# Kernel tuning notes

Measured on AMD Instinct MI355X. Metric: run time of the kernel, lower is better.

Reference implementation:

```python
import jax, jax.numpy as jnp
import numpy as np

EPS = 1e-5

def _conv(x, w, pad):
    # NCHW conv, stride 1, no bias
    return jax.lax.conv_general_dilated(x, w, (1, 1), [(pad, pad), (pad, pad)],
                                        dimension_numbers=('NCHW', 'OIHW', 'NCHW'))

def _bn(x, g, b, m, v):
    # inference-mode BatchNorm2d folded to scale/shift
    s = g * jax.lax.rsqrt(v + EPS)
    return x * s[None, :, None, None] + (b - m * s)[None, :, None, None]

def _cbr(x, w, g, b, m, v):
    # convolution helper module: 3x3 conv (pad 1, no bias) + BN + ReLU
    return jax.nn.relu(_bn(_conv(x, w, 1), g, b, m, v))


def setup_inputs() -> dict:
    key = jax.random.key(0)
    ks = iter(jax.random.split(key, 40))
    dim, mid, B, H, W = 256, 128, 4, 128, 128
    def conv_w(shape):
        fan = shape[1] * shape[2] * shape[3]
        return jax.random.normal(next(ks), shape, jnp.float32) / np.float32(np.sqrt(fan))
    def bn_p(c):
        return (jax.random.normal(next(ks), (c,), jnp.float32) * 0.1 + 1.0,
                jax.random.normal(next(ks), (c,), jnp.float32) * 0.1,
                jax.random.normal(next(ks), (c,), jnp.float32) * 0.1,
                jax.random.uniform(next(ks), (c,), jnp.float32, 0.5, 1.5))
    x = jax.random.normal(next(ks), (B, dim, H, W), jnp.float32)
    w_p1 = conv_w((mid, dim, 3, 3)); g_p1, b_p1, m_p1, v_p1 = bn_p(mid)
    w_p2 = conv_w((mid, dim, 3, 3)); g_p2, b_p2, m_p2, v_p2 = bn_p(mid)
    w_pc = conv_w((dim, mid, 3, 3)); g_pb, b_pb, m_pb, v_pb = bn_p(dim)
    w_c1 = conv_w((dim, dim, 1, 1)); g_b1, b_b1, m_b1, v_b1 = bn_p(dim)
    w_c2 = conv_w((dim, dim, 3, 3)); g_c2, b_c2, m_c2, v_c2 = bn_p(dim)
    return dict(x=x,
                w_p1=w_p1, g_p1=g_p1, b_p1=b_p1, m_p1=m_p1, v_p1=v_p1,
                w_p2=w_p2, g_p2=g_p2, b_p2=b_p2, m_p2=m_p2, v_p2=v_p2,
                w_pc=w_pc, g_pb=g_pb, b_pb=b_pb, m_pb=m_pb, v_pb=v_pb,
                w_c1=w_c1, g_b1=g_b1, b_b1=b_b1, m_b1=m_b1, v_b1=v_b1,
                w_c2=w_c2, g_c2=g_c2, b_c2=b_c2, m_c2=m_c2, v_c2=v_c2)


def reference(x, w_p1, g_p1, b_p1, m_p1, v_p1,
              w_p2, g_p2, b_p2, m_p2, v_p2,
              w_pc, g_pb, b_pb, m_pb, v_pb,
              w_c1, g_b1, b_b1, m_b1, v_b1,
              w_c2, g_c2, b_c2, m_c2, v_c2):
    p1 = _cbr(x, w_p1, g_p1, b_p1, m_p1, v_p1)          # [B,128,H,W]
    top = jax.lax.cummax(p1, axis=2, reverse=True)       # TopPool: max over rows below
    p2 = _cbr(x, w_p2, g_p2, b_p2, m_p2, v_p2)          # [B,128,H,W]
    left = jax.lax.cummax(p2, axis=3, reverse=True)      # LeftPool: max over cols to the right
    p_bn1 = _bn(_conv(top + left, w_pc, 1), g_pb, b_pb, m_pb, v_pb)  # [B,dim,H,W]
    bn1 = _bn(_conv(x, w_c1, 0), g_b1, b_b1, m_b1, v_b1)             # 1x1 skip branch
    relu1 = jax.nn.relu(p_bn1 + bn1)
    return _cbr(relu1, w_c2, g_c2, b_c2, m_c2, v_c2)
```

## Files before the change

kernel.cpp:

```cpp
#include <hip/hip_runtime.h>
#include <hip/hip_bf16.h>

#define HH 128
#define WW 128
#define BB 4
#define NPIX 16384
#define EPSV 1e-5f

using bfrag = __attribute__((ext_vector_type(8))) short;
using f32x4 = __attribute__((ext_vector_type(4))) float;
using us8   = __attribute__((ext_vector_type(8))) unsigned short;

__device__ __forceinline__ float bf2f(ushort u) {
  union { unsigned int i; float f; } x; x.i = ((unsigned int)u) << 16; return x.f;
}
__device__ __forceinline__ ushort f2bf(float f) {
  union { float f; unsigned int i; } x; x.f = f;
  unsigned int r = x.i + 0x7fffu + ((x.i >> 16) & 1u);
  return (ushort)(r >> 16);
}

#define GLOAD16(gsrc, ldst) \
  __builtin_amdgcn_global_load_lds( \
      (const __attribute__((address_space(1))) unsigned int*)(gsrc), \
      (__attribute__((address_space(3))) unsigned int*)(ldst), 16, 0, 0)

template<int CIN1, int TAPS1, int CIN2, int TAPS2, int EPI>
__global__ __launch_bounds__(512, 2)
void convgemm(const ushort* __restrict__ B1,
              const ushort* __restrict__ B2,
              const ushort* __restrict__ wR,
              const float*  __restrict__ tb,
              const float*  __restrict__ tb2,
              void*          __restrict__ outp,
              const ushort* __restrict__ zerop)
{
  __shared__ char ldsb[131072];
  constexpr int nch1 = CIN1 / 64;
  constexpr int nch2 = (CIN2 > 0) ? CIN2 / 64 : 0;
  constexpr int NCH  = TAPS1 * nch1 + TAPS2 * nch2;

  const int nid = (blockIdx.x & 7) * 32 + (blockIdx.x >> 3);
  const int b   = nid >> 6;
  const int h2  = (nid & 63) * 2;

  const int tid  = threadIdx.x;
  const int lane = tid & 63;
  const int wid  = tid >> 6;
  const int wc   = wid & 3;
  const int m0   = (wid >> 2) * 128;
  const int n0   = wc * 64;

  f32x4 acc[8][4];
  #pragma unroll
  for (int i = 0; i < 8; ++i)
    #pragma unroll
    for (int j = 0; j < 4; ++j) acc[i][j] = (f32x4){0.f, 0.f, 0.f, 0.f};

  const int sl8 = (((tid & 7) ^ ((tid >> 3) & 7)) << 3);
  int ro1[4], ro2[4], w_[4], prow_[4];
  #pragma unroll
  for (int s = 0; s < 4; ++s) {
    const int rowB = s * 64 + (tid >> 3);
    prow_[s] = rowB >> 7;
    w_[s]    = rowB & 127;
    ro1[s]   = (prow_[s] * WW + w_[s]) * CIN1 + sl8;
    ro2[s]   = (CIN2 > 0) ? rowB * CIN2 + sl8 : 0;
  }
  const size_t B1base = (size_t)b * NPIX * CIN1;
  const size_t B2base = (CIN2 > 0) ? (size_t)b * NPIX * CIN2 : 0;

  auto stageB = [&](int t, int buf) {
    char* base = ldsb + buf * 65536 + 32768;
    if (CIN2 == 0 || t < TAPS1 * nch1) {
      const int tap = t / nch1, ch = t - tap * nch1;
      const int dy = (TAPS1 == 9) ? tap / 3 - 1 : 0;
      const int dx = (TAPS1 == 9) ? tap - (tap / 3) * 3 - 1 : 0;
      const int hy0 = h2 + dy;
      const bool oob0 = (hy0 < 0) | (hy0 > 127);
      const bool oob1 = (hy0 + 1 < 0) | (hy0 + 1 > 127);
      const int zr = (dx < 0) ? 0 : ((dx > 0) ? 127 : -1);
      const ushort* bch = B1 + B1base + (size_t)(hy0 * WW + dx) * CIN1 + ch * 64;
      #pragma unroll
      for (int s = 0; s < 4; ++s) {
        const bool bad = (prow_[s] ? oob1 : oob0) || (w_[s] == zr);
        const ushort* src = bad ? zerop : (bch + ro1[s]);
        GLOAD16(src, base + s * 8192 + tid * 16);
      }
    } else {
      const int ch = t - TAPS1 * nch1;
      const ushort* bch = B2 + B2base + (size_t)(h2 * WW) * CIN2 + ch * 64;
      #pragma unroll
      for (int s = 0; s < 4; ++s)
        GLOAD16(bch + ro2[s], base + s * 8192 + tid * 16);
    }
  };

  auto stageA = [&](int t, int buf) {
    char* base = ldsb + buf * 65536;
    const char* wsrc = (const char*)(wR + (size_t)t * (256 * 64));
    GLOAD16(wsrc + 0 * 8192 + tid * 16, base + 0 * 8192 + tid * 16);
    GLOAD16(wsrc + 2 * 8192 + tid * 16, base + 2 * 8192 + tid * 16);
    GLOAD16(wsrc + 1 * 8192 + tid * 16, base + 1 * 8192 + tid * 16);
    GLOAD16(wsrc + 3 * 8192 + tid * 16, base + 3 * 8192 + tid * 16);
  };

  stageB(0, 0);
  stageA(0, 0);
  int cur = 0;
  for (int t = 0; t < NCH; ++t) {
    const char* cbase = ldsb + cur * 65536;
    asm volatile("s_waitcnt vmcnt(2)" ::: "memory");
    __builtin_amdgcn_s_barrier();
    __builtin_amdgcn_sched_barrier(0);
    bfrag bf[2][4], af[2][4];
    #pragma unroll
    for (int kc = 0; kc < 2; ++kc) {
      const int sw = ((((kc << 2) | (lane >> 4)) ^ (lane & 7)) << 4);
      #pragma unroll
      for (int nf = 0; nf < 4; ++nf)
        bf[kc][nf] = *(const bfrag*)(cbase + 32768 +
                        (n0 + nf * 16 + (lane & 15)) * 128 + sw);
      #pragma unroll
      for (int mf = 0; mf < 4; ++mf)
        af[kc][mf] = *(const bfrag*)(cbase +
                        (m0 + mf * 16 + (lane & 15)) * 128 + sw);
    }
    if (t + 1 < NCH) stageB(t + 1, cur ^ 1);
    __builtin_amdgcn_s_setprio(1);
    #pragma unroll
    for (int kc = 0; kc < 2; ++kc)
      #pragma unroll
      for (int mf = 0; mf < 4; ++mf)
        #pragma unroll
        for (int nf = 0; nf < 4; ++nf)
          acc[mf][nf] = __builtin_amdgcn_mfma_f32_16x16x32_bf16(
              af[kc][mf], bf[kc][nf], acc[mf][nf], 0, 0, 0);
    __builtin_amdgcn_s_setprio(0);
    __builtin_amdgcn_sched_barrier(0);
    if (t + 1 < NCH) asm volatile("s_waitcnt vmcnt(4)" ::: "memory");
    else             asm volatile("s_waitcnt vmcnt(0)" ::: "memory");
    __builtin_amdgcn_s_barrier();
    __builtin_amdgcn_sched_barrier(0);
    bfrag ag[2][4];
    #pragma unroll
    for (int kc = 0; kc < 2; ++kc) {
      const int sw = ((((kc << 2) | (lane >> 4)) ^ (lane & 7)) << 4);
      #pragma unroll
      for (int mf = 0; mf < 4; ++mf)
        ag[kc][mf] = *(const bfrag*)(cbase +
                        (m0 + 64 + mf * 16 + (lane & 15)) * 128 + sw);
    }
    if (t + 1 < NCH) stageA(t + 1, cur ^ 1);
    __builtin_amdgcn_s_setprio(1);
    #pragma unroll
    for (int kc = 0; kc < 2; ++kc)
      #pragma unroll
      for (int mf = 0; mf < 4; ++mf)
        #pragma unroll
        for (int nf = 0; nf < 4; ++nf)
          acc[4 + mf][nf] = __builtin_amdgcn_mfma_f32_16x16x32_bf16(
              ag[kc][mf], bf[kc][nf], acc[4 + mf][nf], 0, 0, 0);
    __builtin_amdgcn_s_setprio(0);
    __builtin_amdgcn_sched_barrier(0);
    cur ^= 1;
  }

  if (EPI == 4) {
    ushort* ct = (ushort*)ldsb;
    #pragma unroll
    for (int ph = 0; ph < 2; ++ph) {
      __syncthreads();
      if ((wc >> 1) == ph) {
        const int lp0 = (wc & 1) * 64 + (lane & 15);
        #pragma unroll
        for (int mf = 0; mf < 8; ++mf) {
          #pragma unroll
          for (int r2 = 0; r2 < 4; ++r2) {
            const int o = m0 + mf * 16 + (lane >> 4) * 4 + r2;
            const float bias = tb[o] + tb2[o];
            #pragma unroll
            for (int nf = 0; nf < 4; ++nf)
              ct[(lp0 + nf * 16) * 264 + o] =
                  f2bf(fmaxf(acc[mf][nf][r2] + bias, 0.f));
          }
        }
      }
      __syncthreads();
      const int lp = tid >> 2;
      const int q  = tid & 3;
      ushort* dst = (ushort*)outp +
          ((size_t)b * NPIX + (h2 + ph) * WW + lp) * 256 + q * 64;
      const ushort* src = ct + lp * 264 + q * 64;
      #pragma unroll
      for (int j = 0; j < 8; ++j)
        *(us8*)(dst + j * 8) = *(const us8*)(src + j * 8);
    }
    return;
  }

  const int prow = wc >> 1;
  const int hout = h2 + prow;
  const int wbase = (wc & 1) * 64 + (lane & 15);
  #pragma unroll
  for (int mf = 0; mf < 8; ++mf) {
    #pragma unroll
    for (int r2 = 0; r2 < 4; ++r2) {
      const int o = m0 + mf * 16 + (lane >> 4) * 4 + r2;
      const float bias = tb[o];
      #pragma unroll
      for (int nf = 0; nf < 4; ++nf) {
        const int w = wbase + nf * 16;
        float v = fmaxf(acc[mf][nf][r2] + bias, 0.f);
        const size_t oi = (((size_t)(b * 256 + o)) << 14) + hout * WW + w;
        if (EPI == 0) ((ushort*)outp)[oi] = f2bf(v);
        else          ((float*)outp)[oi] = v;
      }
    }
  }
}

struct WSeg {
  const float *W, *g, *bb, *mm, *vv;
  ushort* dst; float* tb;
  int CIN, COUT, TAPS, o_off, cb, start, end;
};

__device__ __forceinline__ void wrepack_one(const WSeg& s, int e) {
  const int tap = e % s.TAPS;
  const int ci  = (e / s.TAPS) % s.CIN;
  const int o   = e / (s.TAPS * s.CIN);
  const int oi  = o + s.o_off;
  const float sc = s.g[o] * rsqrtf(s.vv[o] + EPSV);
  const int nch = s.CIN / 64;
  const int ch = ci >> 6, kl = ci & 63;
  const int slot = (kl >> 3) ^ (oi & 7);
  s.dst[(((size_t)((s.cb + tap * nch + ch) * s.COUT) + oi) << 6) +
        (slot << 3) + (kl & 7)] = f2bf(s.W[e] * sc);
  if (ci == 0 && tap == 0) s.tb[oi] = s.bb[o] - s.mm[o] * sc;
}

__global__ __launch_bounds__(256)
void wrepack_all(WSeg s0, WSeg s1, WSeg s2, WSeg s3, WSeg s4) {
  const int id = blockIdx.x * 256 + threadIdx.x;
  if (id < s0.end)      wrepack_one(s0, id - s0.start);
  else if (id < s1.end) wrepack_one(s1, id - s1.start);
  else if (id < s2.end) wrepack_one(s2, id - s2.start);
  else if (id < s3.end) wrepack_one(s3, id - s3.start);
  else if (id < s4.end) wrepack_one(s4, id - s4.start);
}

__global__ __launch_bounds__(256)
void repack_x(const float* __restrict__ x, ushort* __restrict__ xT)
{
  const int b  = blockIdx.z;
  const int cq = threadIdx.x >> 6;
  const int pg = threadIdx.x & 63;
  const int p0 = blockIdx.x * 256 + pg * 4;
  const size_t xb = (size_t)b * 256 * NPIX;
  ushort* ob = xT + ((size_t)b * NPIX + p0) * 256 + cq * 64;
  for (int cc = 0; cc < 64; cc += 8) {
    us8 v[4];
    #pragma unroll
    for (int j = 0; j < 8; ++j) {
      const float4 q = *(const float4*)&x[xb + (size_t)(cq * 64 + cc + j) * NPIX + p0];
      v[0][j] = f2bf(q.x); v[1][j] = f2bf(q.y);
      v[2][j] = f2bf(q.z); v[3][j] = f2bf(q.w);
    }
    #pragma unroll
    for (int k = 0; k < 4; ++k)
      *(us8*)(ob + (size_t)k * 256 + cc) = v[k];
  }
}

__global__ __launch_bounds__(256)
void sum_repack(const ushort* __restrict__ p12, ushort* __restrict__ sT)
{
  const int b  = blockIdx.z;
  const int cq = threadIdx.x >> 6;
  const int pg = threadIdx.x & 63;
  const int p0 = blockIdx.x * 256 + pg * 4;
  const size_t base = (size_t)b * 256 * NPIX;
  const ushort* P1 = p12 + base;
  const ushort* P2 = p12 + base + (size_t)128 * NPIX;
  ushort* ob = sT + ((size_t)b * NPIX + p0) * 128 + cq * 32;
  for (int cc = 0; cc < 32; cc += 8) {
    us8 v[4];
    #pragma unroll
    for (int j = 0; j < 8; ++j) {
      const size_t ci = (size_t)(cq * 32 + cc + j) * NPIX + p0;
      const ushort4 a = *(const ushort4*)&P1[ci];
      const ushort4 d = *(const ushort4*)&P2[ci];
      v[0][j] = f2bf(bf2f(a.x) + bf2f(d.x));
      v[1][j] = f2bf(bf2f(a.y) + bf2f(d.y));
      v[2][j] = f2bf(bf2f(a.z) + bf2f(d.z));
      v[3][j] = f2bf(bf2f(a.w) + bf2f(d.w));
    }
    #pragma unroll
    for (int k = 0; k < 4; ++k)
      *(us8*)(ob + (size_t)k * 128 + cc) = v[k];
  }
}

__global__ __launch_bounds__(256)
void scans(ushort* __restrict__ p)
{
  const int bid = blockIdx.x;
  if (bid < 256) {
    const int b = bid >> 6;
    const int c = (bid & 63) * 2 + (threadIdx.x >> 7);
    const int w = threadIdx.x & 127;
    ushort* base = p + ((size_t)(b * 256 + c)) * NPIX + w;
    float cur = bf2f(base[(HH - 1) * WW]);
    for (int hr = HH - 2; hr >= 0; --hr) {
      cur = fmaxf(cur, bf2f(base[hr * WW]));
      base[hr * WW] = f2bf(cur);
    }
  } else {
    const int lane = threadIdx.x & 63;
    const int rid  = (bid - 256) * 4 + (threadIdx.x >> 6);
    const int b = rid >> 14;
    const int rem = rid & 16383;
    const int c = rem >> 7, h = rem & 127;
    ushort* r = p + ((size_t)(b * 256 + 128 + c)) * NPIX + h * WW;
    const ushort2 u = ((const ushort2*)r)[lane];
    const float e0 = bf2f(u.x), e1 = bf2f(u.y);
    float m = fmaxf(e0, e1);
    #pragma unroll
    for (int off = 1; off < 64; off <<= 1) {
      const float o = __shfl_down(m, off, 64);
      if (lane + off < 64) m = fmaxf(m, o);
    }
    float s = __shfl_down(m, 1, 64);
    if (lane == 63) s = -3.4e38f;
    const float o1 = fmaxf(e1, s);
    const float o0 = fmaxf(e0, o1);
    ushort2 w2; w2.x = f2bf(o0); w2.y = f2bf(o1);
    ((ushort2*)r)[lane] = w2;
  }
}

extern "C" void kernel_launch(void* const* d_in, const int* in_sizes, int n_in,
                              void* d_out, int out_size, void* d_ws, size_t ws_size,
                              hipStream_t stream) {
  const float* x    = (const float*)d_in[0];
  const float* w_p1 = (const float*)d_in[1];
  const float* g_p1 = (const float*)d_in[2];
  const float* b_p1 = (const float*)d_in[3];
  const float* m_p1 = (const float*)d_in[4];
  const float* v_p1 = (const float*)d_in[5];
  const float* w_p2 = (const float*)d_in[6];
  const float* g_p2 = (const float*)d_in[7];
  const float* b_p2 = (const float*)d_in[8];
  const float* m_p2 = (const float*)d_in[9];
  const float* v_p2 = (const float*)d_in[10];
  const float* w_pc = (const float*)d_in[11];
  const float* g_pb = (const float*)d_in[12];
  const float* b_pb = (const float*)d_in[13];
  const float* m_pb = (const float*)d_in[14];
  const float* v_pb = (const float*)d_in[15];
  const float* w_c1 = (const float*)d_in[16];
  const float* g_b1 = (const float*)d_in[17];
  const float* b_b1 = (const float*)d_in[18];
  const float* m_b1 = (const float*)d_in[19];
  const float* v_b1 = (const float*)d_in[20];
  const float* w_c2 = (const float*)d_in[21];
  const float* g_c2 = (const float*)d_in[22];
  const float* b_c2 = (const float*)d_in[23];
  const float* m_c2 = (const float*)d_in[24];
  const float* v_c2 = (const float*)d_in[25];

  char* ws = (char*)d_ws;
  ushort* xT      = (ushort*)(ws + 0);
  ushort* p12     = (ushort*)(ws + 33554432);
  ushort* relu1T  = (ushort*)(ws + 33554432);
  ushort* sumT    = (ushort*)(ws + 67108864);
  ushort* wR_p12  = (ushort*)(ws + 100663296);
  ushort* wR_pcc1 = (ushort*)(ws + 101842944);
  ushort* wR_c2   = (ushort*)(ws + 102563840);
  float*  tb_p12  = (float*)(ws + 103743488);
  float*  tb_pc   = (float*)(ws + 103744512);
  float*  tb_c1   = (float*)(ws + 103745536);
  float*  tb_c2   = (float*)(ws + 103746560);
  ushort* zerop   = (ushort*)(ws + 103747584);

  hipMemsetAsync(zerop, 0, 256, stream);

  const int n_p  = 128 * 256 * 9;
  const int n_pc = 256 * 128 * 9;
  const int n_c1 = 256 * 256 * 1;
  const int n_c2 = 256 * 256 * 9;
  WSeg s0 = {w_p1, g_p1, b_p1, m_p1, v_p1, wR_p12, tb_p12, 256, 256, 9, 0, 0,
             0, n_p};
  WSeg s1 = {w_p2, g_p2, b_p2, m_p2, v_p2, wR_p12, tb_p12, 256, 256, 9, 128, 0,
             n_p, 2 * n_p};
  WSeg s2 = {w_pc, g_pb, b_pb, m_pb, v_pb, wR_pcc1, tb_pc, 128, 256, 9, 0, 0,
             2 * n_p, 2 * n_p + n_pc};
  WSeg s3 = {w_c1, g_b1, b_b1, m_b1, v_b1, wR_pcc1, tb_c1, 256, 256, 1, 0, 18,
             2 * n_p + n_pc, 2 * n_p + n_pc + n_c1};
  WSeg s4 = {w_c2, g_c2, b_c2, m_c2, v_c2, wR_c2, tb_c2, 256, 256, 9, 0, 0,
             2 * n_p + n_pc + n_c1, 2 * n_p + n_pc + n_c1 + n_c2};
  const int n_all = 2 * n_p + n_pc + n_c1 + n_c2;
  wrepack_all<<<dim3((n_all + 255) / 256), 256, 0, stream>>>(s0, s1, s2, s3, s4);

  repack_x<<<dim3(NPIX / 256, 1, BB), 256, 0, stream>>>(x, xT);

  convgemm<256, 9, 0, 0, 0><<<dim3(256), 512, 0, stream>>>(
      xT, nullptr, wR_p12, tb_p12, nullptr, p12, zerop);

  scans<<<dim3(256 + 16384), 256, 0, stream>>>(p12);

  sum_repack<<<dim3(NPIX / 256, 1, BB), 256, 0, stream>>>(p12, sumT);

  convgemm<128, 9, 256, 1, 4><<<dim3(256), 512, 0, stream>>>(
      sumT, xT, wR_pcc1, tb_pc, tb_c1, relu1T, zerop);

  convgemm<256, 9, 0, 0, 3><<<dim3(256), 512, 0, stream>>>(
      relu1T, nullptr, wR_c2, tb_c2, nullptr, (void*)d_out, zerop);
}
```

Before: 287.1 us.

## Split GEMM main loop into four phases with finer-grained interleaved prefetch

The per-chunk loop is restructured from two halves into four phases (A-half by k-chunk). Each phase reads only the LDS fragments it needs and issues half of the next chunk's global-to-LDS staging between phases. Wait counts are retuned so each phase waits only on the segments it reads. The intent is to overlap global loads with MFMA work more evenly and cut register pressure from holding fragments. The cost is more barriers per iteration, and the correctness of the vmcnt accounting depends on the order in which segments are loaded.

```diff
diff --git a/kernel.cpp b/kernel.cpp
--- a/kernel.cpp
+++ b/kernel.cpp
@@ -70,7 +70,7 @@
   const size_t B1base = (size_t)b * NPIX * CIN1;
   const size_t B2base = (CIN2 > 0) ? (size_t)b * NPIX * CIN2 : 0;
 
-  auto stageB = [&](int t, int buf) {
+  auto stageB = [&](int t, int buf, int part) {
     char* base = ldsb + buf * 65536 + 32768;
     if (CIN2 == 0 || t < TAPS1 * nch1) {
       const int tap = t / nch1, ch = t - tap * nch1;
@@ -82,7 +82,8 @@
       const int zr = (dx < 0) ? 0 : ((dx > 0) ? 127 : -1);
       const ushort* bch = B1 + B1base + (size_t)(hy0 * WW + dx) * CIN1 + ch * 64;
       #pragma unroll
-      for (int s = 0; s < 4; ++s) {
+      for (int si = 0; si < 2; ++si) {
+        const int s = part * 2 + si;
         const bool bad = (prow_[s] ? oob1 : oob0) || (w_[s] == zr);
         const ushort* src = bad ? zerop : (bch + ro1[s]);
         GLOAD16(src, base + s * 8192 + tid * 16);
@@ -91,80 +92,95 @@
       const int ch = t - TAPS1 * nch1;
       const ushort* bch = B2 + B2base + (size_t)(h2 * WW) * CIN2 + ch * 64;
       #pragma unroll
-      for (int s = 0; s < 4; ++s)
+      for (int si = 0; si < 2; ++si) {
+        const int s = part * 2 + si;
         GLOAD16(bch + ro2[s], base + s * 8192 + tid * 16);
+      }
     }
   };
 
-  auto stageA = [&](int t, int buf) {
+  auto stageA = [&](int t, int buf, int part) {
     char* base = ldsb + buf * 65536;
     const char* wsrc = (const char*)(wR + (size_t)t * (256 * 64));
-    GLOAD16(wsrc + 0 * 8192 + tid * 16, base + 0 * 8192 + tid * 16);
-    GLOAD16(wsrc + 2 * 8192 + tid * 16, base + 2 * 8192 + tid * 16);
-    GLOAD16(wsrc + 1 * 8192 + tid * 16, base + 1 * 8192 + tid * 16);
-    GLOAD16(wsrc + 3 * 8192 + tid * 16, base + 3 * 8192 + tid * 16);
+    const int sa = part, sb = part + 2;
+    GLOAD16(wsrc + sa * 8192 + tid * 16, base + sa * 8192 + tid * 16);
+    GLOAD16(wsrc + sb * 8192 + tid * 16, base + sb * 8192 + tid * 16);
   };
 
-  stageB(0, 0);
-  stageA(0, 0);
+#define READ_A(dst_, mfh_, kc_) do { \
+    const int sw_ = ((((kc_) << 2) | (lane >> 4)) ^ (lane & 7)) << 4; \
+    _Pragma("unroll") \
+    for (int mf_ = 0; mf_ < 4; ++mf_) \
+      dst_[mf_] = *(const bfrag*)(cbase + \
+          (m0 + (mfh_) * 64 + mf_ * 16 + (lane & 15)) * 128 + sw_); \
+  } while (0)
+
+#define READ_B(dst_, kc_) do { \
+    const int sw_ = ((((kc_) << 2) | (lane >> 4)) ^ (lane & 7)) << 4; \
+    _Pragma("unroll") \
+    for (int nf_ = 0; nf_ < 4; ++nf_) \
+      dst_[nf_] = *(const bfrag*)(cbase + 32768 + \
+          (n0 + nf_ * 16 + (lane & 15)) * 128 + sw_); \
+  } while (0)
+
+#define MFMA16(rb_, A_, B_) do { \
+    __builtin_amdgcn_s_setprio(1); \
+    _Pragma("unroll") \
+    for (int mf_ = 0; mf_ < 4; ++mf_) \
+      _Pragma("unroll") \
+      for (int nf_ = 0; nf_ < 4; ++nf_) \
+        acc[(rb_) + mf_][nf_] = __builtin_amdgcn_mfma_f32_16x16x32_bf16( \
+            A_[mf_], B_[nf_], acc[(rb_) + mf_][nf_], 0, 0, 0); \
+    __builtin_amdgcn_s_setprio(0); \
+  } while (0)
+
+  stageB(0, 0, 0);
+  stageB(0, 0, 1);
+  stageA(0, 0, 0);
+  stageA(0, 0, 1);
   int cur = 0;
   for (int t = 0; t < NCH; ++t) {
     const char* cbase = ldsb + cur * 65536;
-    asm volatile("s_waitcnt vmcnt(2)" ::: "memory");
-    __builtin_amdgcn_s_barrier();
-    __builtin_amdgcn_sched_barrier(0);
-    bfrag bf[2][4], af[2][4];
-    #pragma unroll
-    for (int kc = 0; kc < 2; ++kc) {
-      const int sw = ((((kc << 2) | (lane >> 4)) ^ (lane & 7)) << 4);
-      #pragma unroll
-      for (int nf = 0; nf < 4; ++nf)
-        bf[kc][nf] = *(const bfrag*)(cbase + 32768 +
-                        (n0 + nf * 16 + (lane & 15)) * 128 + sw);
-      #pragma unroll
-      for (int mf = 0; mf < 4; ++mf)
-        af[kc][mf] = *(const bfrag*)(cbase +
-                        (m0 + mf * 16 + (lane & 15)) * 128 + sw);
-    }
-    if (t + 1 < NCH) stageB(t + 1, cur ^ 1);
-    __builtin_amdgcn_s_setprio(1);
-    #pragma unroll
-    for (int kc = 0; kc < 2; ++kc)
-      #pragma unroll
-      for (int mf = 0; mf < 4; ++mf)
-        #pragma unroll
-        for (int nf = 0; nf < 4; ++nf)
-          acc[mf][nf] = __builtin_amdgcn_mfma_f32_16x16x32_bf16(
-              af[kc][mf], bf[kc][nf], acc[mf][nf], 0, 0, 0);
-    __builtin_amdgcn_s_setprio(0);
-    __builtin_amdgcn_sched_barrier(0);
-    if (t + 1 < NCH) asm volatile("s_waitcnt vmcnt(4)" ::: "memory");
-    else             asm volatile("s_waitcnt vmcnt(0)" ::: "memory");
-    __builtin_amdgcn_s_barrier();
-    __builtin_amdgcn_sched_barrier(0);
-    bfrag ag[2][4];
-    #pragma unroll
-    for (int kc = 0; kc < 2; ++kc) {
-      const int sw = ((((kc << 2) | (lane >> 4)) ^ (lane & 7)) << 4);
-      #pragma unroll
-      for (int mf = 0; mf < 4; ++mf)
-        ag[kc][mf] = *(const bfrag*)(cbase +
-                        (m0 + 64 + mf * 16 + (lane & 15)) * 128 + sw);
-    }
-    if (t + 1 < NCH) stageA(t + 1, cur ^ 1);
-    __builtin_amdgcn_s_setprio(1);
-    #pragma unroll
-    for (int kc = 0; kc < 2; ++kc)
-      #pragma unroll
-      for (int mf = 0; mf < 4; ++mf)
-        #pragma unroll
-        for (int nf = 0; nf < 4; ++nf)
-          acc[4 + mf][nf] = __builtin_amdgcn_mfma_f32_16x16x32_bf16(
-              ag[kc][mf], bf[kc][nf], acc[4 + mf][nf], 0, 0, 0);
-    __builtin_amdgcn_s_setprio(0);
-    __builtin_amdgcn_sched_barrier(0);
+    const bool pf = (t + 1 < NCH);
+    if (pf) stageB(t + 1, cur ^ 1, 0);
+    if (pf) asm volatile("s_waitcnt vmcnt(4)" ::: "memory");
+    else    asm volatile("s_waitcnt vmcnt(2)" ::: "memory");
+    __builtin_amdgcn_s_barrier();
+    __builtin_amdgcn_sched_barrier(0);
+    bfrag bf0[4], af0[4];
+    READ_B(bf0, 0);
+    READ_A(af0, 0, 0);
+    __builtin_amdgcn_sched_barrier(0);
+    __builtin_amdgcn_s_barrier();
+    MFMA16(0, af0, bf0);
+    if (pf) stageB(t + 1, cur ^ 1, 1);
+    if (pf) asm volatile("s_waitcnt vmcnt(4)" ::: "memory");
+    else    asm volatile("s_waitcnt vmcnt(0)" ::: "memory");
+    __builtin_amdgcn_s_barrier();
+    __builtin_amdgcn_sched_barrier(0);
+    bfrag af1[4];
+    READ_A(af1, 1, 0);
+    __builtin_amdgcn_sched_barrier(0);
+    __builtin_amdgcn_s_barrier();
+    MFMA16(4, af1, bf0);
+    if (pf) stageA(t + 1, cur ^ 1, 0);
+    bfrag bf1[4], af2[4];
+    READ_B(bf1, 1);
+    READ_A(af2, 0, 1);
+    __builtin_amdgcn_sched_barrier(0);
+    __builtin_amdgcn_s_barrier();
+    MFMA16(0, af2, bf1);
+    if (pf) stageA(t + 1, cur ^ 1, 1);
+    bfrag af3[4];
+    READ_A(af3, 1, 1);
+    __builtin_amdgcn_sched_barrier(0);
+    __builtin_amdgcn_s_barrier();
+    MFMA16(4, af3, bf1);
     cur ^= 1;
   }
+#undef READ_A
+#undef READ_B
+#undef MFMA16
 
   if (EPI == 4) {
     ushort* ct = (ushort*)ldsb;
```

Result: no change. 290.8 us (+1.3%).

## Restructure conv GEMM to 4 waves with 128x128 per-wave tiles and simpler pipeline

Applied to the files above, without the earlier changes.

The conv GEMM kernel goes from 8 waves (512 threads, 128x64 per wave) to 4 waves (256 threads, 128x128 per wave, 64 accumulators each). The staggered split A/B staging with partial vmcnt waits is replaced by one stage per K-chunk, a full vmcnt(0) wait and a single barrier, followed by all MFMAs. Each wave gets more register reuse and fewer barriers per chunk, but far more VGPRs (256 accumulator floats). It also loses the overlap that the split-phase waits gave, and latency hiding drops with fewer waves.

```diff
diff --git a/kernel.cpp b/kernel.cpp
--- a/kernel.cpp
+++ b/kernel.cpp
@@ -26,7 +26,7 @@
       (__attribute__((address_space(3))) unsigned int*)(ldst), 16, 0, 0)
 
 template<int CIN1, int TAPS1, int CIN2, int TAPS2, int EPI>
-__global__ __launch_bounds__(512, 2)
+__global__ __launch_bounds__(256, 1)
 void convgemm(const ushort* __restrict__ B1,
               const ushort* __restrict__ B2,
               const ushort* __restrict__ wR,
@@ -47,31 +47,36 @@
   const int tid  = threadIdx.x;
   const int lane = tid & 63;
   const int wid  = tid >> 6;
-  const int wc   = wid & 3;
-  const int m0   = (wid >> 2) * 128;
-  const int n0   = wc * 64;
-
-  f32x4 acc[8][4];
+  const int m0   = (wid >> 1) * 128;
+  const int n0   = (wid & 1) * 128;
+
+  f32x4 acc[8][8];
   #pragma unroll
   for (int i = 0; i < 8; ++i)
     #pragma unroll
-    for (int j = 0; j < 4; ++j) acc[i][j] = (f32x4){0.f, 0.f, 0.f, 0.f};
-
-  const int sl8 = (((tid & 7) ^ ((tid >> 3) & 7)) << 3);
-  int ro1[4], ro2[4], w_[4], prow_[4];
+    for (int j = 0; j < 8; ++j) acc[i][j] = (f32x4){0.f, 0.f, 0.f, 0.f};
+
+  int ro1[8], ro2[8], w_[8], prow_[8];
   #pragma unroll
-  for (int s = 0; s < 4; ++s) {
-    const int rowB = s * 64 + (tid >> 3);
+  for (int s = 0; s < 8; ++s) {
+    const int boff = s * 4096 + tid * 16;
+    const int rowB = boff >> 7;
     prow_[s] = rowB >> 7;
     w_[s]    = rowB & 127;
-    ro1[s]   = (prow_[s] * WW + w_[s]) * CIN1 + sl8;
-    ro2[s]   = (CIN2 > 0) ? rowB * CIN2 + sl8 : 0;
+    const int sl8 = (((tid & 7) ^ (rowB & 7)) << 3);
+    ro1[s] = (prow_[s] * WW + w_[s]) * CIN1 + sl8;
+    ro2[s] = (CIN2 > 0) ? rowB * CIN2 + sl8 : 0;
   }
   const size_t B1base = (size_t)b * NPIX * CIN1;
   const size_t B2base = (CIN2 > 0) ? (size_t)b * NPIX * CIN2 : 0;
 
-  auto stageB = [&](int t, int buf) {
-    char* base = ldsb + buf * 65536 + 32768;
+  auto stage = [&](int t, int buf) {
+    char* baseA = ldsb + buf * 65536;
+    char* baseB = baseA + 32768;
+    const char* wsrc = (const char*)(wR + (size_t)t * (256 * 64));
+    #pragma unroll
+    for (int i = 0; i < 8; ++i)
+      GLOAD16(wsrc + i * 4096 + tid * 16, baseA + i * 4096 + tid * 16);
     if (CIN2 == 0 || t < TAPS1 * nch1) {
       const int tap = t / nch1, ch = t - tap * nch1;
       const int dy = (TAPS1 == 9) ? tap / 3 - 1 : 0;
@@ -82,88 +87,47 @@
       const int zr = (dx < 0) ? 0 : ((dx > 0) ? 127 : -1);
       const ushort* bch = B1 + B1base + (size_t)(hy0 * WW + dx) * CIN1 + ch * 64;
       #pragma unroll
-      for (int s = 0; s < 4; ++s) {
+      for (int s = 0; s < 8; ++s) {
         const bool bad = (prow_[s] ? oob1 : oob0) || (w_[s] == zr);
         const ushort* src = bad ? zerop : (bch + ro1[s]);
-        GLOAD16(src, base + s * 8192 + tid * 16);
+        GLOAD16(src, baseB + s * 4096 + tid * 16);
       }
     } else {
       const int ch = t - TAPS1 * nch1;
       const ushort* bch = B2 + B2base + (size_t)(h2 * WW) * CIN2 + ch * 64;
       #pragma unroll
-      for (int s = 0; s < 4; ++s)
-        GLOAD16(bch + ro2[s], base + s * 8192 + tid * 16);
+      for (int s = 0; s < 8; ++s)
+        GLOAD16(bch + ro2[s], baseB + s * 4096 + tid * 16);
     }
   };
 
-  auto stageA = [&](int t, int buf) {
-    char* base = ldsb + buf * 65536;
-    const char* wsrc = (const char*)(wR + (size_t)t * (256 * 64));
-    GLOAD16(wsrc + 0 * 8192 + tid * 16, base + 0 * 8192 + tid * 16);
-    GLOAD16(wsrc + 2 * 8192 + tid * 16, base + 2 * 8192 + tid * 16);
-    GLOAD16(wsrc + 1 * 8192 + tid * 16, base + 1 * 8192 + tid * 16);
-    GLOAD16(wsrc + 3 * 8192 + tid * 16, base + 3 * 8192 + tid * 16);
-  };
-
-  stageB(0, 0);
-  stageA(0, 0);
-  int cur = 0;
+  stage(0, 0);
   for (int t = 0; t < NCH; ++t) {
-    const char* cbase = ldsb + cur * 65536;
-    asm volatile("s_waitcnt vmcnt(2)" ::: "memory");
+    asm volatile("s_waitcnt vmcnt(0)" ::: "memory");
     __builtin_amdgcn_s_barrier();
     __builtin_amdgcn_sched_barrier(0);
-    bfrag bf[2][4], af[2][4];
+    if (t + 1 < NCH) stage(t + 1, (t + 1) & 1);
+    const char* cb = ldsb + (t & 1) * 65536;
     #pragma unroll
     for (int kc = 0; kc < 2; ++kc) {
       const int sw = ((((kc << 2) | (lane >> 4)) ^ (lane & 7)) << 4);
-      #pragma unroll
-      for (int nf = 0; nf < 4; ++nf)
-        bf[kc][nf] = *(const bfrag*)(cbase + 32768 +
-                        (n0 + nf * 16 + (lane & 15)) * 128 + sw);
-      #pragma unroll
-      for (int mf = 0; mf < 4; ++mf)
-        af[kc][mf] = *(const bfrag*)(cbase +
-                        (m0 + mf * 16 + (lane & 15)) * 128 + sw);
-    }
-    if (t + 1 < NCH) stageB(t + 1, cur ^ 1);
-    __builtin_amdgcn_s_setprio(1);
-    #pragma unroll
-    for (int kc = 0; kc < 2; ++kc)
-      #pragma unroll
-      for (int mf = 0; mf < 4; ++mf)
+      bfrag af[8], bf[8];
+      #pragma unroll
+      for (int mf = 0; mf < 8; ++mf)
+        af[mf] = *(const bfrag*)(cb + (m0 + mf * 16 + (lane & 15)) * 128 + sw);
+      #pragma unroll
+      for (int nf = 0; nf < 8; ++nf)
+        bf[nf] = *(const bfrag*)(cb + 32768 +
+                     (n0 + nf * 16 + (lane & 15)) * 128 + sw);
+      __builtin_amdgcn_s_setprio(1);
+      #pragma unroll
+      for (int mf = 0; mf < 8; ++mf)
         #pragma unroll
-        for (int nf = 0; nf < 4; ++nf)
+        for (int nf = 0; nf < 8; ++nf)
           acc[mf][nf] = __builtin_amdgcn_mfma_f32_16x16x32_bf16(
-              af[kc][mf], bf[kc][nf], acc[mf][nf], 0, 0, 0);
-    __builtin_amdgcn_s_setprio(0);
-    __builtin_amdgcn_sched_barrier(0);
-    if (t + 1 < NCH) asm volatile("s_waitcnt vmcnt(4)" ::: "memory");
-    else             asm volatile("s_waitcnt vmcnt(0)" ::: "memory");
-    __builtin_amdgcn_s_barrier();
-    __builtin_amdgcn_sched_barrier(0);
-    bfrag ag[2][4];
-    #pragma unroll
-    for (int kc = 0; kc < 2; ++kc) {
-      const int sw = ((((kc << 2) | (lane >> 4)) ^ (lane & 7)) << 4);
-      #pragma unroll
-      for (int mf = 0; mf < 4; ++mf)
-        ag[kc][mf] = *(const bfrag*)(cbase +
-                        (m0 + 64 + mf * 16 + (lane & 15)) * 128 + sw);
-    }
-    if (t + 1 < NCH) stageA(t + 1, cur ^ 1);
-    __builtin_amdgcn_s_setprio(1);
-    #pragma unroll
-    for (int kc = 0; kc < 2; ++kc)
-      #pragma unroll
-      for (int mf = 0; mf < 4; ++mf)
-        #pragma unroll
-        for (int nf = 0; nf < 4; ++nf)
-          acc[4 + mf][nf] = __builtin_amdgcn_mfma_f32_16x16x32_bf16(
-              ag[kc][mf], bf[kc][nf], acc[4 + mf][nf], 0, 0, 0);
-    __builtin_amdgcn_s_setprio(0);
-    __builtin_amdgcn_sched_barrier(0);
-    cur ^= 1;
+              af[mf], bf[nf], acc[mf][nf], 0, 0, 0);
+      __builtin_amdgcn_s_setprio(0);
+    }
   }
 
   if (EPI == 4) {
@@ -171,8 +135,7 @@
     #pragma unroll
     for (int ph = 0; ph < 2; ++ph) {
       __syncthreads();
-      if ((wc >> 1) == ph) {
-        const int lp0 = (wc & 1) * 64 + (lane & 15);
+      if ((wid & 1) == ph) {
         #pragma unroll
         for (int mf = 0; mf < 8; ++mf) {
           #pragma unroll
@@ -180,28 +143,25 @@
             const int o = m0 + mf * 16 + (lane >> 4) * 4 + r2;
             const float bias = tb[o] + tb2[o];
             #pragma unroll
-            for (int nf = 0; nf < 4; ++nf)
-              ct[(lp0 + nf * 16) * 264 + o] =
+            for (int nf = 0; nf < 8; ++nf)
+              ct[(nf * 16 + (lane & 15)) * 264 + o] =
                   f2bf(fmaxf(acc[mf][nf][r2] + bias, 0.f));
           }
         }
       }
       __syncthreads();
-      const int lp = tid >> 2;
-      const int q  = tid & 3;
+      const int p  = tid >> 1;
+      const int hf = tid & 1;
       ushort* dst = (ushort*)outp +
-          ((size_t)b * NPIX + (h2 + ph) * WW + lp) * 256 + q * 64;
-      const ushort* src = ct + lp * 264 + q * 64;
-      #pragma unroll
-      for (int j = 0; j < 8; ++j)
+          ((size_t)b * NPIX + (h2 + ph) * WW + p) * 256 + hf * 128;
+      const ushort* src = ct + p * 264 + hf * 128;
+      #pragma unroll
+      for (int j = 0; j < 16; ++j)
         *(us8*)(dst + j * 8) = *(const us8*)(src + j * 8);
     }
     return;
   }
 
-  const int prow = wc >> 1;
-  const int hout = h2 + prow;
-  const int wbase = (wc & 1) * 64 + (lane & 15);
   #pragma unroll
   for (int mf = 0; mf < 8; ++mf) {
     #pragma unroll
@@ -209,8 +169,10 @@
       const int o = m0 + mf * 16 + (lane >> 4) * 4 + r2;
       const float bias = tb[o];
       #pragma unroll
-      for (int nf = 0; nf < 4; ++nf) {
-        const int w = wbase + nf * 16;
+      for (int nf = 0; nf < 8; ++nf) {
+        const int px   = n0 + nf * 16 + (lane & 15);
+        const int hout = h2 + (px >> 7);
+        const int w    = px & 127;
         float v = fmaxf(acc[mf][nf][r2] + bias, 0.f);
         const size_t oi = (((size_t)(b * 256 + o)) << 14) + hout * WW + w;
         if (EPI == 0) ((ushort*)outp)[oi] = f2bf(v);
@@ -405,16 +367,16 @@
 
   repack_x<<<dim3(NPIX / 256, 1, BB), 256, 0, stream>>>(x, xT);
 
-  convgemm<256, 9, 0, 0, 0><<<dim3(256), 512, 0, stream>>>(
+  convgemm<256, 9, 0, 0, 0><<<dim3(256), 256, 0, stream>>>(
       xT, nullptr, wR_p12, tb_p12, nullptr, p12, zerop);
 
   scans<<<dim3(256 + 16384), 256, 0, stream>>>(p12);
 
   sum_repack<<<dim3(NPIX / 256, 1, BB), 256, 0, stream>>>(p12, sumT);
 
-  convgemm<128, 9, 256, 1, 4><<<dim3(256), 512, 0, stream>>>(
+  convgemm<128, 9, 256, 1, 4><<<dim3(256), 256, 0, stream>>>(
       sumT, xT, wR_pcc1, tb_pc, tb_c1, relu1T, zerop);
 
-  convgemm<256, 9, 0, 0, 3><<<dim3(256), 512, 0, stream>>>(
+  convgemm<256, 9, 0, 0, 3><<<dim3(256), 256, 0, stream>>>(
       relu1T, nullptr, wR_c2, tb_c2, nullptr, (void*)d_out, zerop);
 }
```

After: 331.5 us. +15.5%, slower.
